# Performance work log

Measured on AMD Instinct MI355X. Metric: run time of the kernel, lower is better.

## Reference

```python
import math
import jax, jax.numpy as jnp
import numpy as np
from jax import lax

G_RATIO = 0.5       # g_ratio init arg
TMAX_RATIO = 0.25


def setup_inputs() -> dict:
    key = jax.random.key(0)
    k1, k2, k3, k4 = jax.random.split(key, 4)
    N = 4096
    cost_maps = jax.random.uniform(k1, (N,), jnp.float32)          # heuristic h(v)
    nodes = jax.random.uniform(k2, (N, 2), jnp.float32)            # coords (only size used)
    adj = (jax.random.uniform(k3, (N, N)) < 0.005).astype(jnp.float32)
    adj = jnp.maximum(adj, adj.T)                                  # symmetric PRM-like graph
    w = jax.random.uniform(k4, (N, N), jnp.float32, minval=0.1, maxval=1.0)
    weighted_adj = adj * w                                         # edge lengths
    return {"start_index": 0, "goal_index": N - 1, "cost_maps": cost_maps,
            "nodes": nodes, "adj": adj, "weighted_adj": weighted_adj}


def _astar_forward(start_index, goal_index, cost_maps, adj, weighted_adj):
    N = cost_maps.shape[0]
    inv_sqrt_n = 1.0 / math.sqrt(N)
    diag = jnp.arange(N)
    adj = adj.at[diag, diag].set(0.0)
    weighted_adj = jnp.where(jnp.isinf(weighted_adj), 0.0, weighted_adj)
    weighted_adj = weighted_adj.at[diag, diag].set(0.0)

    h = cost_maps
    goal_maps = jnp.zeros((N,), cost_maps.dtype).at[goal_index].set(1.0)
    open0 = jnp.zeros((N,), cost_maps.dtype).at[start_index].set(1.0)
    hist0 = jnp.zeros((N,), cost_maps.dtype)
    g0 = weighted_adj[start_index]
    parents0 = jnp.full((N,), float(goal_index), cost_maps.dtype)
    Tmax = int(TMAX_RATIO * N)  # training-mode budget

    def step(carry, t):
        open_m, hist, g, parents, done, t_final = carry
        f = G_RATIO * g + (1.0 - G_RATIO) * h
        f_exp = jnp.exp(-f * inv_sqrt_n) * open_m
        denom = jnp.sum(f_exp)
        y = f_exp / jnp.where(denom == 0.0, 1.0, denom)  # guard only hits after done
        ind = jnp.argmax(y)
        y_hard = jnp.zeros_like(y).at[ind].set(1.0)
        snm = lax.stop_gradient(y_hard - y) + y  # straight-through one-hot select
        solved = jnp.sum(snm * goal_maps) >= 1e-8
        open2 = jnp.clip(open_m - snm, 0.0, 1.0)
        hist2 = jnp.clip(hist + snm, 0.0, 1.0)
        neighbor = (snm @ adj) * (1.0 - open2) * (1.0 - hist2)   # row-gather via matvec
        g2 = g[ind] + weighted_adj[ind]                          # tentative g through ind
        idx = lax.stop_gradient(((1.0 - open2) * (1.0 - hist2) + open2 * (g > g2).astype(g.dtype)) * neighbor)
        g_new = lax.stop_gradient(g2 * idx + g * (1.0 - idx))
        open3 = lax.stop_gradient(jnp.clip(open2 + idx, 0.0, 1.0))
        parents_new = ind.astype(parents.dtype) * idx + parents * (1.0 - idx)
        keep = done  # freeze state after goal found (mimics torch break)
        carry_out = (jnp.where(keep, open_m, open3),
                     jnp.where(keep, hist, hist2),
                     jnp.where(keep, g, g_new),
                     jnp.where(keep, parents, parents_new),
                     done | solved,
                     jnp.where(keep, t_final, t))
        return carry_out, None

    init = (open0, hist0, g0, parents0, jnp.array(False), jnp.int32(0))
    (open_m, hist, g, parents, done, t_final), _ = lax.scan(
        step, init, jnp.arange(Tmax, dtype=jnp.int32))

    # backtrack: path_maps[loc]=1; loc=parents[loc], repeated t_final times
    parents_i = parents.astype(jnp.int32)
    path0 = goal_maps.astype(jnp.int32)
    loc0 = parents_i[goal_index]

    def bt(carry, i):
        path, loc = carry
        do = i < t_final
        path = jnp.where(do, path.at[loc].set(1), path)
        loc = jnp.where(do, parents_i[loc], loc)
        return (path, loc), None

    (path_maps, _), _ = lax.scan(bt, (path0, loc0), jnp.arange(Tmax, dtype=jnp.int32))
    return hist, path_maps


def reference(start_index, goal_index, cost_maps, nodes, adj, weighted_adj):
    # training-mode forward: returns (histories, path_maps)
    return _astar_forward(start_index, goal_index, cost_maps, adj, weighted_adj)
```

## Files before the change

kernel.cpp:

```cpp
#include <hip/hip_runtime.h>
#include <math.h>


#define NN    4096
#define TMAXI 1024
#define CAP   96
#define STR   104

__device__ __forceinline__ float clip01(float x) {
    return fminf(fmaxf(x, 0.0f), 1.0f);
}

__device__ __forceinline__ float fexp_of(float g, float h, float open) {
    float f = __fadd_rn(__fmul_rn(0.5f, g), __fmul_rn(0.5f, h));
    return __fmul_rn(expf(__fmul_rn(-f, 0.015625f)), open);
}

template <int CTRL, int RMASK>
__device__ __forceinline__ double dpp_mov_d(double x) {
    int lo = __double2loint(x), hi = __double2hiint(x);
    lo = __builtin_amdgcn_update_dpp(lo, lo, CTRL, RMASK, 0xf, false);
    hi = __builtin_amdgcn_update_dpp(hi, hi, CTRL, RMASK, 0xf, false);
    return __hiloint2double(hi, lo);
}

__device__ __forceinline__ double wave_max_f64(double x) {
    x = fmax(x, dpp_mov_d<0x111, 0xf>(x));
    x = fmax(x, dpp_mov_d<0x112, 0xf>(x));
    x = fmax(x, dpp_mov_d<0x114, 0xf>(x));
    x = fmax(x, dpp_mov_d<0x118, 0xf>(x));
    x = fmax(x, dpp_mov_d<0x142, 0xa>(x));
    x = fmax(x, dpp_mov_d<0x143, 0xc>(x));
    int lo = __builtin_amdgcn_readlane(__double2loint(x), 63);
    int hi = __builtin_amdgcn_readlane(__double2hiint(x), 63);
    return __hiloint2double(hi, lo);
}

__global__ __launch_bounds__(256)
void build_csr(const float* __restrict__ wadj, float2* __restrict__ ent)
{
    __shared__ int lcnt;
    const int r = blockIdx.x;
    if (threadIdx.x == 0) lcnt = 0;
    __syncthreads();
    const float4* wrow = (const float4*)(wadj + (size_t)r * NN);
    for (int c = 0; c < NN / (256 * 4); ++c) {
        int t4 = c * 256 + threadIdx.x;
        float4 w4 = wrow[t4];
        float wv[4] = {w4.x, w4.y, w4.z, w4.w};
        #pragma unroll
        for (int k = 0; k < 4; ++k) {
            int col = t4 * 4 + k;
            float w = wv[k];
            if (col != r && w != 0.0f && !isinf(w)) {
                int p = atomicAdd(&lcnt, 1);
                if (p < CAP)
                    ent[(size_t)r * STR + 1 + p] =
                        make_float2(__int_as_float(col), w);
            }
        }
    }
    __syncthreads();
    if (threadIdx.x == 0)
        ent[(size_t)r * STR] = make_float2(__int_as_float(min(lcnt, CAP)), 0.0f);
}

__global__ __launch_bounds__(128, 1)
void astar_fwd6(const int* __restrict__ start_p,
                const int* __restrict__ goal_p,
                const float* __restrict__ cost_maps,
                const float* __restrict__ wadj,
                const float2* __restrict__ ent,
                float* __restrict__ scratch,
                float* __restrict__ out)
{
    __shared__ __align__(16) unsigned long long ls_key[NN];
    __shared__ __align__(16) float ls_g[NN];
    __shared__ __align__(16) float ls_par[NN];
    __shared__ __align__(16) float ls_h[NN];
    __shared__ __align__(16) unsigned long long ls_bm[64];

    const int tid = threadIdx.x;

    if (tid >= 64) {
        const float4* p = (const float4*)ent;
        const int total = NN * (STR / 2);
        float acc = 0.0f;
        int l = tid - 64;
        #pragma unroll 4
        for (int i = l; i < total; i += 64) acc += p[i].x;
        scratch[l] = acc;
        return;
    }

    const int lane  = tid;
    const int start = start_p[0];
    const int goal  = goal_p[0];

    {
        const float4* c4 = (const float4*)cost_maps;
        const float4* w4 = (const float4*)(wadj + (size_t)start * NN);
        for (int c = 0; c < NN / (64 * 4); ++c) {
            int j4 = c * 64 + lane;
            float4 hv4 = c4[j4];
            float4 gv4 = w4[j4];
            if (start >= j4 * 4 && start < j4 * 4 + 4)
                ((float*)&gv4)[start - j4 * 4] = 0.0f;
            ((float4*)ls_h)[j4] = hv4;
            ((float4*)ls_g)[j4] = gv4;
            float gf = (float)goal;
            ((float4*)ls_par)[j4] = make_float4(gf, gf, gf, gf);
        }
        for (int c = 0; c < (int)(NN * sizeof(unsigned long long) /
                                  (64 * sizeof(float4))); ++c)
            ((float4*)ls_key)[c * 64 + lane] = make_float4(0.f, 0.f, 0.f, 0.f);
        ls_bm[lane] = 0ull;
        if (lane == 0) {
            float fe = fexp_of(0.0f, ls_h[start], 1.0f);
            double kd = (double)__float_as_uint(fe) * 4096.0
                      + (double)(4095 - start);
            unsigned long long kb = (unsigned long long)__double_as_longlong(kd);
            ls_key[start] = kb;
            ls_bm[start >> 6] = kb;
        }
    }

    int ind = start;
    unsigned long long closedm = 0ull;
    int tf = 0;

    for (int t = 0; t < TMAXI; ++t) {
        const int b = ind >> 6;

        double bm_v = __longlong_as_double((long long)ls_bm[lane]);
        double kb_v = __longlong_as_double(
                          (long long)ls_key[(b << 6) + lane]);
        float  gind = ls_g[ind];
        const float2* row = ent + (size_t)ind * STR;
        float2 hdr = row[0];
        float2 e0  = row[1 + lane];
        float2 e1  = make_float2(0.0f, 0.0f);
        if (lane < 32) e1 = row[65 + lane];

        double kx = kb_v;
        if (lane == (ind & 63)) kx = 0.0;
        if (kx < 2.0) kx = 0.0;
        double K_b = wave_max_f64(kx);

        if (lane == 0) {
            ls_key[ind] = 0x3FF0000000000000ull;
            ls_bm[b] = (unsigned long long)__double_as_longlong(K_b);
        }
        if (lane == b) closedm |= (1ull << (ind & 63));

        const int   cnt  = __float_as_int(hdr.x);
        const float indf = (float)ind;
        double nk = 0.0;

        #pragma unroll
        for (int slot = 0; slot < 2; ++slot) {
            int e = lane + slot * 64;
            float2 ev = slot ? e1 : e0;
            if (e < cnt) {
                int j = __float_as_int(ev.x);
                unsigned long long kj = ls_key[j];
                float hj = ls_h[j];
                if (kj == 0ull) {
                    float g2 = __fadd_rn(gind, ev.y);
                    float fe = fexp_of(g2, hj, 1.0f);
                    double kd = (double)__float_as_uint(fe) * 4096.0
                              + (double)(4095 - j);
                    unsigned long long kb =
                        (unsigned long long)__double_as_longlong(kd);
                    ls_g[j]   = g2;
                    ls_par[j] = indf;
                    ls_key[j] = kb;
                    atomicMax(&ls_bm[j >> 6], kb);
                    nk = fmax(nk, kd);
                }
            }
        }

        tf = t;
        if (ind == goal) break;

        double pv = (lane == b) ? K_b : bm_v;
        double M = wave_max_f64(fmax(pv, nk));
        int ind_next;
        if (M < 2.0) {
            ind_next = 0;
        } else {
            double q   = trunc(M * (1.0 / 4096.0));
            double rem = fma(q, -4096.0, M);
            ind_next = 4095 - (int)rem;
        }
        ind = __builtin_amdgcn_readfirstlane(ind_next);
    }

    ls_bm[lane] = closedm;
    for (int c = 0; c < NN / (64 * 4); ++c)
        ((float4*)ls_h)[c * 64 + lane] = make_float4(0.f, 0.f, 0.f, 0.f);
    if (lane == 0) {
        ls_h[goal] = 1.0f;
        int loc = (int)ls_par[goal];
        for (int i = 0; i < tf; ++i) {
            if (ls_h[loc] != 0.0f) break;
            ls_h[loc] = 1.0f;
            loc = (int)ls_par[loc];
        }
    }
    for (int c = 0; c < NN / (64 * 4); ++c) {
        int j4 = c * 64 + lane;
        unsigned long long m = ls_bm[j4 >> 4];
        unsigned int bits = (unsigned int)(m >> ((j4 & 15) * 4)) & 0xFu;
        float4 hist4;
        hist4.x = (bits & 1u) ? 1.0f : 0.0f;
        hist4.y = (bits & 2u) ? 1.0f : 0.0f;
        hist4.z = (bits & 4u) ? 1.0f : 0.0f;
        hist4.w = (bits & 8u) ? 1.0f : 0.0f;
        ((float4*)out)[j4]        = hist4;
        ((float4*)(out + NN))[j4] = ((const float4*)ls_h)[j4];
    }
}

__global__ __launch_bounds__(1024, 1)
void astar_fwd(const int* __restrict__ start_p,
               const int* __restrict__ goal_p,
               const float* __restrict__ cost_maps,
               const float* __restrict__ adj,
               const float* __restrict__ wadj,
               float* __restrict__ out)
{
    __shared__ __align__(16) float ls_open[NN];
    __shared__ __align__(16) float ls_hist[NN];
    __shared__ __align__(16) float ls_g[NN];
    __shared__ __align__(16) float ls_par[NN];
    __shared__ __align__(16) float ls_fe[NN];
    __shared__ __align__(16) float ls_h[NN];
    __shared__ float red_v[16];
    __shared__ float red_s[16];
    __shared__ int   red_i[16];
    __shared__ float bc_snm, bc_gind;
    __shared__ int   bc_ind, ls_done, ls_tf;

    const int tid   = threadIdx.x;
    const int start = start_p[0];
    const int goal  = goal_p[0];

    for (int k = 0; k < 4; ++k) {
        int j = tid * 4 + k;
        float hv = cost_maps[j];
        float gv = wadj[(size_t)start * NN + j];
        if (j == start) gv = 0.0f;
        float ov = (j == start) ? 1.0f : 0.0f;
        ls_h[j] = hv; ls_g[j] = gv; ls_open[j] = ov;
        ls_hist[j] = 0.0f; ls_par[j] = (float)goal;
        ls_fe[j] = fexp_of(gv, hv, ov);
    }
    if (tid == 0) { ls_done = 0; ls_tf = 0; }
    __syncthreads();

    for (int t = 0; t < TMAXI; ++t) {
        float4 fe4 = *(const float4*)&ls_fe[tid * 4];
        float v0 = fe4.x, v1 = fe4.y, v2 = fe4.z, v3 = fe4.w;
        float sum = ((v0 + v1) + v2) + v3;
        float best = v0; int bi = tid * 4;
        if (v1 > best) { best = v1; bi = tid * 4 + 1; }
        if (v2 > best) { best = v2; bi = tid * 4 + 2; }
        if (v3 > best) { best = v3; bi = tid * 4 + 3; }
        #pragma unroll
        for (int off = 32; off > 0; off >>= 1) {
            float ov = __shfl_down(best, off);
            int   oi = __shfl_down(bi, off);
            float os = __shfl_down(sum, off);
            sum += os;
            if (ov > best || (ov == best && oi < bi)) { best = ov; bi = oi; }
        }
        if ((tid & 63) == 0) {
            int w = tid >> 6;
            red_v[w] = best; red_s[w] = sum; red_i[w] = bi;
        }
        __syncthreads();
        if (tid == 0) {
            float denom = red_s[0]; best = red_v[0]; bi = red_i[0];
            #pragma unroll
            for (int w = 1; w < 16; ++w) {
                denom += red_s[w];
                if (red_v[w] > best || (red_v[w] == best && red_i[w] < bi)) {
                    best = red_v[w]; bi = red_i[w];
                }
            }
            int ind = bi;
            float dg = (denom == 0.0f) ? 1.0f : denom;
            float y_ind = ls_fe[ind] / dg;
            float snm = __fadd_rn(__fsub_rn(1.0f, y_ind), y_ind);
            ls_open[ind] = clip01(__fsub_rn(ls_open[ind], snm));
            ls_hist[ind] = clip01(__fadd_rn(ls_hist[ind], snm));
            ls_fe[ind]   = fexp_of(ls_g[ind], ls_h[ind], ls_open[ind]);
            bc_ind = ind; bc_snm = snm; bc_gind = ls_g[ind];
            ls_tf = t;
            if (ind == goal && snm >= 1e-8f) ls_done = 1;
        }
        __syncthreads();
        {
            const int   ind  = bc_ind;
            const float snm  = bc_snm;
            const float gind = bc_gind;
            const float indf = (float)ind;
            float4 a4 = ((const float4*)(adj  + (size_t)ind * NN))[tid];
            float4 w4 = ((const float4*)(wadj + (size_t)ind * NN))[tid];
            float av[4] = {a4.x, a4.y, a4.z, a4.w};
            float wvv[4] = {w4.x, w4.y, w4.z, w4.w};
            #pragma unroll
            for (int k = 0; k < 4; ++k) {
                int j = tid * 4 + k;
                float a = av[k], w = wvv[k];
                if (j == ind) { a = 0.0f; w = 0.0f; }
                if (a != 0.0f) {
                    float o = ls_open[j], hi = ls_hist[j], gj = ls_g[j];
                    float one_o = __fsub_rn(1.0f, o);
                    float one_h = __fsub_rn(1.0f, hi);
                    float sm    = __fmul_rn(snm, a);
                    float neigh = __fmul_rn(__fmul_rn(sm, one_o), one_h);
                    float g2    = __fadd_rn(gind, w);
                    float cmp   = (gj > g2) ? 1.0f : 0.0f;
                    float s   = __fadd_rn(__fmul_rn(one_o, one_h),
                                          __fmul_rn(o, cmp));
                    float idx = __fmul_rn(s, neigh);
                    if (idx != 0.0f) {
                        float omi = __fsub_rn(1.0f, idx);
                        float gn = __fadd_rn(__fmul_rn(g2, idx),
                                             __fmul_rn(gj, omi));
                        float on = clip01(__fadd_rn(o, idx));
                        float pn = __fadd_rn(__fmul_rn(indf, idx),
                                             __fmul_rn(ls_par[j], omi));
                        ls_g[j] = gn; ls_open[j] = on; ls_par[j] = pn;
                        ls_fe[j] = fexp_of(gn, ls_h[j], on);
                    }
                }
            }
        }
        __syncthreads();
        if (ls_done) break;
    }

    for (int k = 0; k < 4; ++k) {
        int j = tid * 4 + k;
        out[j] = ls_hist[j];
        out[NN + j] = (j == goal) ? 1.0f : 0.0f;
    }
    __syncthreads();
    if (tid == 0) {
        int tfv = ls_tf;
        int loc = (int)ls_par[goal];
        for (int i = 0; i < tfv; ++i) {
            out[NN + loc] = 1.0f;
            loc = (int)ls_par[loc];
        }
    }
}

extern "C" void kernel_launch(void* const* d_in, const int* in_sizes, int n_in,
                              void* d_out, int out_size, void* d_ws, size_t ws_size,
                              hipStream_t stream)
{
    const int*   start_p = (const int*)d_in[0];
    const int*   goal_p  = (const int*)d_in[1];
    const float* cost    = (const float*)d_in[2];
    const float* adj     = (const float*)d_in[4];
    const float* wadj    = (const float*)d_in[5];
    float* out = (float*)d_out;

    const size_t csr_bytes = (size_t)NN * STR * sizeof(float2);
    const size_t need = csr_bytes + 64 * sizeof(float);
    if (ws_size >= need) {
        float2* ent     = (float2*)d_ws;
        float*  scratch = (float*)((char*)d_ws + csr_bytes);
        build_csr<<<dim3(NN), dim3(256), 0, stream>>>(wadj, ent);
        astar_fwd6<<<dim3(1), dim3(128), 0, stream>>>(start_p, goal_p, cost,
                                                      wadj, ent, scratch, out);
    } else {
        astar_fwd<<<dim3(1), dim3(1024), 0, stream>>>(start_p, goal_p, cost,
                                                      adj, wadj, out);
    }
}
```

Before: 649.4 us.

## Speculatively prefetch CSR row of second-best open node each A* step

Each iteration now computes the second-largest open key alongside the maximum and prefetches that node's CSR adjacency row from global memory. When the next selected node matches the speculated one, the row load is skipped, taking global latency off the serial critical path. The g and parent arrays are merged into one float2 LDS array, and the helper warming wave now sweeps the CSR buffer twice. The cost is an extra wave reduction and a global load every step that may be wasted when the speculation misses.

Result: slower. 859.7 us (+32.4%).

```diff
diff --git a/kernel.cpp b/kernel.cpp
--- a/kernel.cpp
+++ b/kernel.cpp
@@ -6,10 +6,6 @@
 #define TMAXI 1024
 #define CAP   96
 #define STR   104
-
-__device__ __forceinline__ float clip01(float x) {
-    return fminf(fmaxf(x, 0.0f), 1.0f);
-}
 
 __device__ __forceinline__ float fexp_of(float g, float h, float open) {
     float f = __fadd_rn(__fmul_rn(0.5f, g), __fmul_rn(0.5f, h));
@@ -34,6 +30,12 @@
     int lo = __builtin_amdgcn_readlane(__double2loint(x), 63);
     int hi = __builtin_amdgcn_readlane(__double2hiint(x), 63);
     return __hiloint2double(hi, lo);
+}
+
+__device__ __forceinline__ int decode_key(double M) {
+    double q   = trunc(M * (1.0 / 4096.0));
+    double rem = fma(q, -4096.0, M);
+    return 4095 - (int)rem;
 }
 
 __global__ __launch_bounds__(256)
@@ -66,7 +68,7 @@
 }
 
 __global__ __launch_bounds__(128, 1)
-void astar_fwd6(const int* __restrict__ start_p,
+void astar_fwd7(const int* __restrict__ start_p,
                 const int* __restrict__ goal_p,
                 const float* __restrict__ cost_maps,
                 const float* __restrict__ wadj,
@@ -75,8 +77,7 @@
                 float* __restrict__ out)
 {
     __shared__ __align__(16) unsigned long long ls_key[NN];
-    __shared__ __align__(16) float ls_g[NN];
-    __shared__ __align__(16) float ls_par[NN];
+    __shared__ __align__(16) float2 ls_gp[NN];
     __shared__ __align__(16) float ls_h[NN];
     __shared__ __align__(16) unsigned long long ls_bm[64];
 
@@ -87,8 +88,9 @@
         const int total = NN * (STR / 2);
         float acc = 0.0f;
         int l = tid - 64;
-        #pragma unroll 4
-        for (int i = l; i < total; i += 64) acc += p[i].x;
+        for (int pass = 0; pass < 2; ++pass)
+            #pragma unroll 4
+            for (int i = l; i < total; i += 64) acc += p[i].x;
         scratch[l] = acc;
         return;
     }
@@ -100,6 +102,7 @@
     {
         const float4* c4 = (const float4*)cost_maps;
         const float4* w4 = (const float4*)(wadj + (size_t)start * NN);
+        const float gf = (float)goal;
         for (int c = 0; c < NN / (64 * 4); ++c) {
             int j4 = c * 64 + lane;
             float4 hv4 = c4[j4];
@@ -107,9 +110,10 @@
             if (start >= j4 * 4 && start < j4 * 4 + 4)
                 ((float*)&gv4)[start - j4 * 4] = 0.0f;
             ((float4*)ls_h)[j4] = hv4;
-            ((float4*)ls_g)[j4] = gv4;
-            float gf = (float)goal;
-            ((float4*)ls_par)[j4] = make_float4(gf, gf, gf, gf);
+            float gv[4] = {gv4.x, gv4.y, gv4.z, gv4.w};
+            #pragma unroll
+            for (int k = 0; k < 4; ++k)
+                ls_gp[j4 * 4 + k] = make_float2(gv[k], gf);
         }
         for (int c = 0; c < (int)(NN * sizeof(unsigned long long) /
                                   (64 * sizeof(float4))); ++c)
@@ -126,21 +130,32 @@
     }
 
     int ind = start;
+    int spec_j = -1;
+    float2 s_hdr = make_float2(0.f, 0.f);
+    float2 s_e0  = make_float2(0.f, 0.f);
+    float2 s_e1  = make_float2(0.f, 0.f);
     unsigned long long closedm = 0ull;
     int tf = 0;
 
     for (int t = 0; t < TMAXI; ++t) {
-        const int b = ind >> 6;
+        const int  b   = ind >> 6;
+        const bool hit = (ind == spec_j);
 
         double bm_v = __longlong_as_double((long long)ls_bm[lane]);
         double kb_v = __longlong_as_double(
                           (long long)ls_key[(b << 6) + lane]);
-        float  gind = ls_g[ind];
-        const float2* row = ent + (size_t)ind * STR;
-        float2 hdr = row[0];
-        float2 e0  = row[1 + lane];
-        float2 e1  = make_float2(0.0f, 0.0f);
-        if (lane < 32) e1 = row[65 + lane];
+        float  gind = ls_gp[ind].x;
+
+        float2 hdr, e0, e1;
+        if (hit) {
+            hdr = s_hdr; e0 = s_e0; e1 = s_e1;
+        } else {
+            const float2* row = ent + (size_t)ind * STR;
+            hdr = row[0];
+            e0  = row[1 + lane];
+            e1  = make_float2(0.0f, 0.0f);
+            if (lane < 32) e1 = row[65 + lane];
+        }
 
         double kx = kb_v;
         if (lane == (ind & 63)) kx = 0.0;
@@ -155,46 +170,68 @@
 
         const int   cnt  = __float_as_int(hdr.x);
         const float indf = (float)ind;
-        double nk = 0.0;
-
-        #pragma unroll
-        for (int slot = 0; slot < 2; ++slot) {
-            int e = lane + slot * 64;
-            float2 ev = slot ? e1 : e0;
-            if (e < cnt) {
-                int j = __float_as_int(ev.x);
-                unsigned long long kj = ls_key[j];
-                float hj = ls_h[j];
-                if (kj == 0ull) {
-                    float g2 = __fadd_rn(gind, ev.y);
-                    float fe = fexp_of(g2, hj, 1.0f);
-                    double kd = (double)__float_as_uint(fe) * 4096.0
-                              + (double)(4095 - j);
-                    unsigned long long kb =
-                        (unsigned long long)__double_as_longlong(kd);
-                    ls_g[j]   = g2;
-                    ls_par[j] = indf;
-                    ls_key[j] = kb;
-                    atomicMax(&ls_bm[j >> 6], kb);
-                    nk = fmax(nk, kd);
-                }
+        double nk0 = 0.0, nk1 = 0.0;
+
+        if (lane < cnt) {
+            int j = __float_as_int(e0.x);
+            unsigned long long kj = ls_key[j];
+            float hj = ls_h[j];
+            if (kj == 0ull) {
+                float g2 = __fadd_rn(gind, e0.y);
+                float fe = fexp_of(g2, hj, 1.0f);
+                double kd = (double)__float_as_uint(fe) * 4096.0
+                          + (double)(4095 - j);
+                unsigned long long kb =
+                    (unsigned long long)__double_as_longlong(kd);
+                ls_gp[j]  = make_float2(g2, indf);
+                ls_key[j] = kb;
+                atomicMax(&ls_bm[j >> 6], kb);
+                nk0 = kd;
+            }
+        }
+        if (lane + 64 < cnt) {
+            int j = __float_as_int(e1.x);
+            unsigned long long kj = ls_key[j];
+            float hj = ls_h[j];
+            if (kj == 0ull) {
+                float g2 = __fadd_rn(gind, e1.y);
+                float fe = fexp_of(g2, hj, 1.0f);
+                double kd = (double)__float_as_uint(fe) * 4096.0
+                          + (double)(4095 - j);
+                unsigned long long kb =
+                    (unsigned long long)__double_as_longlong(kd);
+                ls_gp[j]  = make_float2(g2, indf);
+                ls_key[j] = kb;
+                atomicMax(&ls_bm[j >> 6], kb);
+                nk1 = kd;
             }
         }
 
         tf = t;
         if (ind == goal) break;
 
-        double pv = (lane == b) ? K_b : bm_v;
-        double M = wave_max_f64(fmax(pv, nk));
-        int ind_next;
-        if (M < 2.0) {
-            ind_next = 0;
-        } else {
-            double q   = trunc(M * (1.0 / 4096.0));
-            double rem = fma(q, -4096.0, M);
-            ind_next = 4095 - (int)rem;
-        }
+        double bmx = (lane == b) ? 0.0 : bm_v;
+        double a0 = fmax(bmx, kx), b0 = fmin(bmx, kx);
+        double a1 = fmax(nk0, nk1), b1 = fmin(nk0, nk1);
+        double l1 = fmax(a0, a1);
+        double l2 = fmax(fmin(a0, a1), fmax(b0, b1));
+
+        double M1 = wave_max_f64(l1);
+        int ind_next = (M1 >= 2.0) ? decode_key(M1) : 0;
         ind = __builtin_amdgcn_readfirstlane(ind_next);
+
+        double c2 = (l1 == M1) ? l2 : l1;
+        double M2 = wave_max_f64(c2);
+        spec_j = -1;
+        if (M2 >= 2.0) {
+            int j2 = decode_key(M2);
+            const float2* rw = ent + (size_t)j2 * STR;
+            s_hdr = rw[0];
+            s_e0  = rw[1 + lane];
+            s_e1  = make_float2(0.0f, 0.0f);
+            if (lane < 32) s_e1 = rw[65 + lane];
+            spec_j = j2;
+        }
     }
 
     ls_bm[lane] = closedm;
@@ -202,11 +239,11 @@
         ((float4*)ls_h)[c * 64 + lane] = make_float4(0.f, 0.f, 0.f, 0.f);
     if (lane == 0) {
         ls_h[goal] = 1.0f;
-        int loc = (int)ls_par[goal];
+        int loc = (int)ls_gp[goal].y;
         for (int i = 0; i < tf; ++i) {
             if (ls_h[loc] != 0.0f) break;
             ls_h[loc] = 1.0f;
-            loc = (int)ls_par[loc];
+            loc = (int)ls_gp[loc].y;
         }
     }
     for (int c = 0; c < NN / (64 * 4); ++c) {
@@ -221,6 +258,10 @@
         ((float4*)out)[j4]        = hist4;
         ((float4*)(out + NN))[j4] = ((const float4*)ls_h)[j4];
     }
+}
+
+__device__ __forceinline__ float clip01(float x) {
+    return fminf(fmaxf(x, 0.0f), 1.0f);
 }
 
 __global__ __launch_bounds__(1024, 1)
@@ -377,7 +418,7 @@
         float2* ent     = (float2*)d_ws;
         float*  scratch = (float*)((char*)d_ws + csr_bytes);
         build_csr<<<dim3(NN), dim3(256), 0, stream>>>(wadj, ent);
-        astar_fwd6<<<dim3(1), dim3(128), 0, stream>>>(start_p, goal_p, cost,
+        astar_fwd7<<<dim3(1), dim3(128), 0, stream>>>(start_p, goal_p, cost,
                                                       wadj, ent, scratch, out);
     } else {
         astar_fwd<<<dim3(1), dim3(1024), 0, stream>>>(start_p, goal_p, cost,
```
